# Kernel tuning notes

Measured on AMD Instinct MI355X. Metric: run time of the kernel, lower is better.

The kernel has to match this reference:

```python
import jax, jax.numpy as jnp
import numpy as np

N_NODES = 100000

def spmm(rows, cols, vals, x):
    # out[r] = sum_e vals[e] * x[cols[e]] for edges with rows[e] == r
    msgs = vals[:, None] * x[cols]            # [E, F]
    return jax.ops.segment_sum(msgs, rows, num_segments=N_NODES)

def setup_inputs() -> dict:
    key = jax.random.key(0)
    ks = jax.random.split(key, 8)
    N, E, F_IN, H, C = N_NODES, 1600000, 128, 128, 64
    x = jax.random.normal(ks[0], (N, F_IN), dtype=jnp.float32)
    edge_rows = jax.random.randint(ks[1], (E,), 0, N, dtype=jnp.int32)
    edge_cols = jax.random.randint(ks[2], (E,), 0, N, dtype=jnp.int32)
    edge_vals = jax.random.uniform(ks[3], (E,), dtype=jnp.float32)
    W1 = jax.random.normal(ks[4], (F_IN, H), dtype=jnp.float32) * (1.0 / np.sqrt(F_IN))
    b1 = jnp.zeros((H,), dtype=jnp.float32)
    W2 = jax.random.normal(ks[5], (H, C), dtype=jnp.float32) * (1.0 / np.sqrt(H))
    b2 = jnp.zeros((C,), dtype=jnp.float32)
    return {"x": x, "edge_rows": edge_rows, "edge_cols": edge_cols,
            "edge_vals": edge_vals, "W1": W1, "b1": b1, "W2": W2, "b2": b2}

def reference(x, edge_rows, edge_cols, edge_vals, W1, b1, W2, b2):
    # Layer 1: spmm(adj, x) then linear, then ReLU (dropout = identity at eval)
    h = spmm(edge_rows, edge_cols, edge_vals, x)   # [N, F_IN]
    h = h @ W1 + b1                                # [N, H]
    h = jax.nn.relu(h)
    # Layer 2
    h = spmm(edge_rows, edge_cols, edge_vals, h)   # [N, H]
    return h @ W2 + b2                             # [N, C]
```

## Files before the change

### kernel.cpp

```cpp
#include <hip/hip_runtime.h>


typedef __attribute__((ext_vector_type(8))) short short8;
typedef __attribute__((ext_vector_type(4))) float floatx4;
typedef __attribute__((ext_vector_type(2))) float floatx2;

#define ELLS 64
#define H2LD 136
#define CURS 16

static __device__ __forceinline__ unsigned short f2bf(float f) {
    unsigned int u = __builtin_bit_cast(unsigned int, f);
    u += 0x7fffu + ((u >> 16) & 1u);
    return (unsigned short)(u >> 16);
}
static __device__ __forceinline__ float bflo(unsigned int u) {
    return __builtin_bit_cast(float, u << 16);
}
static __device__ __forceinline__ float bfhi(unsigned int u) {
    return __builtin_bit_cast(float, u & 0xffff0000u);
}
static __device__ __forceinline__ float slotval(unsigned int s) {
    return (float)(s >> 17) * (1.0f / 32767.0f);
}

__global__ __launch_bounds__(256) void prep_kernel(
    const float* __restrict__ W1, const float* __restrict__ W2,
    unsigned short* __restrict__ W1t, unsigned short* __restrict__ W2t,
    int* __restrict__ cursor, int N)
{
    int idx = blockIdx.x * 256 + threadIdx.x;
    int stride = gridDim.x * 256;
    for (int i = idx; i < N * CURS; i += stride) cursor[i] = 0;
    if (idx < 128 * 128) {
        int n = idx >> 7, k = idx & 127;
        W1t[idx] = f2bf(W1[(size_t)k * 128 + n]);
    }
    if (idx < 64 * 128) {
        int n = idx >> 7, k = idx & 127;
        W2t[idx] = f2bf(W2[(size_t)k * 64 + n]);
    }
}

static __device__ __forceinline__ void gemm1_body(
    const float* __restrict__ A, const unsigned short* __restrict__ Wt,
    unsigned short* __restrict__ Y, int N, int bid)
{
    const int lane = threadIdx.x & 63;
    const int wave = threadIdx.x >> 6;
    const int quad = lane >> 4;
    const int l16  = lane & 15;
    const int row0 = bid * 64 + wave * 16;
    int arow = row0 + l16;
    if (arow > N - 1) arow = N - 1;

    short8 af[4];
    const float* ap = A + (size_t)arow * 128 + quad * 8;
    #pragma unroll
    for (int kt = 0; kt < 4; ++kt) {
        const floatx4* p = (const floatx4*)(ap + kt * 32);
        floatx4 lo = __builtin_nontemporal_load(p);
        floatx4 hi = __builtin_nontemporal_load(p + 1);
        short8 t;
        t[0] = (short)f2bf(lo[0]); t[1] = (short)f2bf(lo[1]);
        t[2] = (short)f2bf(lo[2]); t[3] = (short)f2bf(lo[3]);
        t[4] = (short)f2bf(hi[0]); t[5] = (short)f2bf(hi[1]);
        t[6] = (short)f2bf(hi[2]); t[7] = (short)f2bf(hi[3]);
        af[kt] = t;
    }

    floatx4 acc[8];
    #pragma unroll
    for (int nt = 0; nt < 8; ++nt) acc[nt] = (floatx4){0.f, 0.f, 0.f, 0.f};

    #pragma unroll
    for (int nt = 0; nt < 8; ++nt) {
        const unsigned short* wp = Wt + (size_t)(nt * 16 + l16) * 128 + quad * 8;
        #pragma unroll
        for (int kt = 0; kt < 4; ++kt) {
            short8 bfr = *(const short8*)(wp + kt * 32);
            acc[nt] = __builtin_amdgcn_mfma_f32_16x16x32_bf16(
                af[kt], bfr, acc[nt], 0, 0, 0);
        }
    }

    #pragma unroll
    for (int nt = 0; nt < 8; ++nt) {
        int col = nt * 16 + l16;
        #pragma unroll
        for (int r = 0; r < 4; ++r) {
            int row = row0 + quad * 4 + r;
            if (row < N)
                Y[(size_t)row * 128 + col] = f2bf(acc[nt][r]);
        }
    }
}

__global__ __launch_bounds__(256) void fill_ell_gemm1_fused(
    const int* __restrict__ erow, const int* __restrict__ ecol,
    const float* __restrict__ eval, int* __restrict__ cursor,
    unsigned int* __restrict__ ell, int E, int FB, int RSTEP,
    const float* __restrict__ x, const unsigned short* __restrict__ W1t,
    unsigned short* __restrict__ y1b, int N)
{
    if ((int)blockIdx.x < FB) {
        const int g     = blockIdx.x & 7;
        const int chunk = blockIdx.x >> 3;
        const int lo = g * RSTEP;
        const int span = min(RSTEP, N - lo);
        int base = chunk * 1024 + (int)threadIdx.x * 4;
        if (base >= E) return;

        if (base + 4 <= E) {
            int4   r4 = *(const int4*)(erow + base);
            int4   c4 = *(const int4*)(ecol + base);
            float4 v4 = *(const float4*)(eval + base);
            int   rr[4] = {r4.x, r4.y, r4.z, r4.w};
            int   cc[4] = {c4.x, c4.y, c4.z, c4.w};
            float vv[4] = {v4.x, v4.y, v4.z, v4.w};
            #pragma unroll
            for (int j = 0; j < 4; ++j) {
                int r = rr[j];
                if ((unsigned)(r - lo) < (unsigned)span) {
                    int p = atomicAdd(&cursor[(size_t)r * CURS], 1);
                    if (p < ELLS) {
                        unsigned int pk = (unsigned int)cc[j]
                            | ((unsigned int)(int)(vv[j] * 32767.f + 0.5f) << 17);
                        ell[((size_t)r << 6) + p] = pk;
                    }
                }
            }
        } else {
            for (int j = 0; j < 4; ++j) {
                int e = base + j;
                if (e < E) {
                    int r = erow[e];
                    if ((unsigned)(r - lo) < (unsigned)span) {
                        int p = atomicAdd(&cursor[(size_t)r * CURS], 1);
                        if (p < ELLS) {
                            unsigned int pk = (unsigned int)ecol[e]
                                | ((unsigned int)(int)(eval[e] * 32767.f + 0.5f) << 17);
                            ell[((size_t)r << 6) + p] = pk;
                        }
                    }
                }
            }
        }
    } else {
        gemm1_body(x, W1t, y1b, N, blockIdx.x - FB);
    }
}

__global__ __launch_bounds__(1024, 8) void spmm128_gemm2_fused(
    const int* __restrict__ deg, const unsigned int* __restrict__ ell,
    const unsigned short* __restrict__ y1b, const float* __restrict__ b1,
    const unsigned short* __restrict__ W2t,
    unsigned short* __restrict__ y2b, int N)
{
    __shared__ unsigned short h2s[16 * H2LD];

    const int wave = threadIdx.x >> 6;
    const int lane = threadIdx.x & 63;
    const int row  = blockIdx.x * 16 + wave;

    unsigned int pack = 0;
    if (row < N) {
        const unsigned int* xf = (const unsigned int*)y1b;
        int d  = min(deg[(size_t)row * CURS], ELLS);
        int d8 = (d + 7) & ~7;
        const unsigned int* ep = ell + ((size_t)row << 6);

        float ax[8], ay[8];
        #pragma unroll
        for (int j = 0; j < 8; ++j) { ax[j] = 0.f; ay[j] = 0.f; }

        for (int i = 0; i < d8; i += 8) {
            uint4 q0 = *(const uint4*)(ep + i);
            uint4 q1 = *(const uint4*)(ep + i + 4);
            unsigned int s[8] = {q0.x, q0.y, q0.z, q0.w,
                                 q1.x, q1.y, q1.z, q1.w};
            unsigned int sv[8];
            unsigned int u[8];
            #pragma unroll
            for (int j = 0; j < 8; ++j) {
                unsigned int ss = (i + j < d) ? s[j] : 0u;
                sv[j] = ss;
                u[j] = xf[((ss & 0x1FFFFu) << 6) | (unsigned)lane];
            }
            #pragma unroll
            for (int j = 0; j < 8; ++j) {
                float vvv = slotval(sv[j]);
                ax[j] = fmaf(vvv, bflo(u[j]), ax[j]);
                ay[j] = fmaf(vvv, bfhi(u[j]), ay[j]);
            }
        }
        float2 b = ((const float2*)b1)[lane];
        float sx = ((ax[0] + ax[1]) + (ax[2] + ax[3]))
                 + ((ax[4] + ax[5]) + (ax[6] + ax[7])) + b.x;
        float sy = ((ay[0] + ay[1]) + (ay[2] + ay[3]))
                 + ((ay[4] + ay[5]) + (ay[6] + ay[7])) + b.y;
        sx = fmaxf(sx, 0.f);
        sy = fmaxf(sy, 0.f);
        pack = (unsigned int)f2bf(sx) | ((unsigned int)f2bf(sy) << 16);
    }
    ((unsigned int*)(h2s + wave * H2LD))[lane] = pack;
    __syncthreads();

    if (wave < 4) {
        const int quad = lane >> 4;
        const int l16  = lane & 15;
        const int nt   = wave;

        short8 af[4];
        #pragma unroll
        for (int kt = 0; kt < 4; ++kt)
            af[kt] = *(const short8*)(h2s + l16 * H2LD + quad * 8 + kt * 32);

        floatx4 acc = (floatx4){0.f, 0.f, 0.f, 0.f};
        const unsigned short* wp = W2t + (size_t)(nt * 16 + l16) * 128 + quad * 8;
        #pragma unroll
        for (int kt = 0; kt < 4; ++kt) {
            short8 bfr = *(const short8*)(wp + kt * 32);
            acc = __builtin_amdgcn_mfma_f32_16x16x32_bf16(af[kt], bfr, acc, 0, 0, 0);
        }

        int col = nt * 16 + l16;
        #pragma unroll
        for (int r = 0; r < 4; ++r) {
            int grow = blockIdx.x * 16 + quad * 4 + r;
            if (grow < N)
                y2b[(size_t)grow * 64 + col] = f2bf(acc[r]);
        }
    }
}

__global__ __launch_bounds__(256) void spmm_gather64_out(
    const int* __restrict__ deg, const unsigned int* __restrict__ ell,
    const unsigned short* __restrict__ y2b,
    const float* __restrict__ bias, float* __restrict__ out, int N)
{
    int row = (blockIdx.x * 256 + threadIdx.x) >> 6;
    if (row >= N) return;
    int lane = threadIdx.x & 63;
    int half = lane >> 5, fl = lane & 31;
    const unsigned int* xf = (const unsigned int*)y2b;

    int d  = min(deg[(size_t)row * CURS], ELLS);
    int d8 = (d + 7) & ~7;
    const unsigned int* ep = ell + ((size_t)row << 6);

    float ax[4], ay[4];
    #pragma unroll
    for (int j = 0; j < 4; ++j) { ax[j] = 0.f; ay[j] = 0.f; }

    for (int i = half * 4; i < d8; i += 8) {
        uint4 q = *(const uint4*)(ep + i);
        unsigned int s[4] = {q.x, q.y, q.z, q.w};
        unsigned int sv[4];
        unsigned int u[4];
        #pragma unroll
        for (int j = 0; j < 4; ++j) {
            unsigned int ss = (i + j < d) ? s[j] : 0u;
            sv[j] = ss;
            u[j] = xf[((ss & 0x1FFFFu) << 5) | (unsigned)fl];
        }
        #pragma unroll
        for (int j = 0; j < 4; ++j) {
            float vvv = slotval(sv[j]);
            ax[j] = fmaf(vvv, bflo(u[j]), ax[j]);
            ay[j] = fmaf(vvv, bfhi(u[j]), ay[j]);
        }
    }
    float sx = (ax[0] + ax[1]) + (ax[2] + ax[3]);
    float sy = (ay[0] + ay[1]) + (ay[2] + ay[3]);
    sx += __shfl_xor(sx, 32);
    sy += __shfl_xor(sy, 32);
    if (half == 0) {
        float2 b = ((const float2*)bias)[fl];
        floatx2 o; o[0] = sx + b.x; o[1] = sy + b.y;
        __builtin_nontemporal_store(o, (floatx2*)out + (size_t)row * 32 + fl);
    }
}

extern "C" void kernel_launch(void* const* d_in, const int* in_sizes, int n_in,
                              void* d_out, int out_size, void* d_ws, size_t ws_size,
                              hipStream_t stream)
{
    const float* x    = (const float*)d_in[0];
    const int*   erow = (const int*)  d_in[1];
    const int*   ecol = (const int*)  d_in[2];
    const float* eval = (const float*)d_in[3];
    const float* W1   = (const float*)d_in[4];
    const float* b1   = (const float*)d_in[5];
    const float* W2   = (const float*)d_in[6];
    const float* b2   = (const float*)d_in[7];
    float*       out  = (float*)d_out;

    const int N = in_sizes[0] / 128;
    const int E = in_sizes[1];
    const int NP = N + 64;

    unsigned short* y1b = (unsigned short*)d_ws;
    unsigned short* y2b = y1b + (size_t)NP * 128;
    unsigned short* W1t = y2b + (size_t)NP * 64;
    unsigned short* W2t = W1t + 128 * 128;
    unsigned int* ell   = (unsigned int*)(W2t + 64 * 128);
    int*   cursor = (int*)(ell + (size_t)N * ELLS);

    const int spmm_blocks  = (N + 3) / 4;
    const int fused_blocks = (N + 15) / 16;
    const int mfma_blocks  = (N + 63) / 64;
    const int prep_blocks  = (N + 255) / 256;
    const int RSTEP        = (N + 7) / 8;
    const int chunks       = (E + 1023) / 1024;
    const int FB           = 8 * chunks;

    prep_kernel<<<prep_blocks, 256, 0, stream>>>(W1, W2, W1t, W2t, cursor, N);

    fill_ell_gemm1_fused<<<FB + mfma_blocks, 256, 0, stream>>>(
        erow, ecol, eval, cursor, ell, E, FB, RSTEP, x, W1t, y1b, N);

    spmm128_gemm2_fused<<<fused_blocks, 1024, 0, stream>>>(
        cursor, ell, y1b, b1, W2t, y2b, N);

    spmm_gather64_out<<<spmm_blocks, 256, 0, stream>>>(
        cursor, ell, y2b, b2, out, N);
}
```

Baseline: 328.5 us.

## Build ELL via two-pass chunk binning with LDS counting sort instead of global atomics

Replaces the ELL fill, which scanned the edge list eight times and did per-edge global atomics on cursors, with a two-pass binning scheme. Pass A sorts each 4096-edge chunk into 256-row buckets with an LDS histogram and prefix scan, and writes a compact slab plus per-chunk offsets. Pass B has one block per bucket assemble that bucket's ELL rows in LDS and write them out coalesced, along with a dense degree array. This also removes zeroing of the padded cursor array. The cost is an extra kernel launch, an intermediate slab round-trip through memory, and a per-bucket loop over all chunks with limited parallelism.

```diff
diff --git a/kernel.cpp b/kernel.cpp
--- a/kernel.cpp
+++ b/kernel.cpp
@@ -7,7 +7,10 @@
 
 #define ELLS 64
 #define H2LD 136
-#define CURS 16
+#define RW   256
+#define CH   4096
+#define EPT  16
+#define MAXB 400
 
 static __device__ __forceinline__ unsigned short f2bf(float f) {
     unsigned int u = __builtin_bit_cast(unsigned int, f);
@@ -26,12 +29,9 @@
 
 __global__ __launch_bounds__(256) void prep_kernel(
     const float* __restrict__ W1, const float* __restrict__ W2,
-    unsigned short* __restrict__ W1t, unsigned short* __restrict__ W2t,
-    int* __restrict__ cursor, int N)
+    unsigned short* __restrict__ W1t, unsigned short* __restrict__ W2t)
 {
     int idx = blockIdx.x * 256 + threadIdx.x;
-    int stride = gridDim.x * 256;
-    for (int i = idx; i < N * CURS; i += stride) cursor[i] = 0;
     if (idx < 128 * 128) {
         int n = idx >> 7, k = idx & 127;
         W1t[idx] = f2bf(W1[(size_t)k * 128 + n]);
@@ -96,59 +96,143 @@
     }
 }
 
-__global__ __launch_bounds__(256) void fill_ell_gemm1_fused(
+__global__ __launch_bounds__(256) void binA_gemm1_fused(
     const int* __restrict__ erow, const int* __restrict__ ecol,
-    const float* __restrict__ eval, int* __restrict__ cursor,
-    unsigned int* __restrict__ ell, int E, int FB, int RSTEP,
+    const float* __restrict__ eval,
+    uint2* __restrict__ slab, unsigned int* __restrict__ offsT,
+    int E, int NC, int NB,
     const float* __restrict__ x, const unsigned short* __restrict__ W1t,
     unsigned short* __restrict__ y1b, int N)
 {
-    if ((int)blockIdx.x < FB) {
-        const int g     = blockIdx.x & 7;
-        const int chunk = blockIdx.x >> 3;
-        const int lo = g * RSTEP;
-        const int span = min(RSTEP, N - lo);
-        int base = chunk * 1024 + (int)threadIdx.x * 4;
-        if (base >= E) return;
-
-        if (base + 4 <= E) {
-            int4   r4 = *(const int4*)(erow + base);
-            int4   c4 = *(const int4*)(ecol + base);
-            float4 v4 = *(const float4*)(eval + base);
-            int   rr[4] = {r4.x, r4.y, r4.z, r4.w};
-            int   cc[4] = {c4.x, c4.y, c4.z, c4.w};
-            float vv[4] = {v4.x, v4.y, v4.z, v4.w};
+    __shared__ unsigned int hist[MAXB + 1];
+    __shared__ uint2 compact[CH];
+
+    if ((int)blockIdx.x < NC) {
+        const int t     = threadIdx.x;
+        const int chunk = blockIdx.x;
+
+        for (int i = t; i <= NB; i += 256) hist[i] = 0;
+        __syncthreads();
+
+        int base = chunk * CH + t * EPT;
+        unsigned int w0[EPT];
+        unsigned int vb[EPT];
+        int bk[EPT], rk[EPT];
+
+        if (base + EPT <= E) {
             #pragma unroll
-            for (int j = 0; j < 4; ++j) {
-                int r = rr[j];
-                if ((unsigned)(r - lo) < (unsigned)span) {
-                    int p = atomicAdd(&cursor[(size_t)r * CURS], 1);
-                    if (p < ELLS) {
-                        unsigned int pk = (unsigned int)cc[j]
-                            | ((unsigned int)(int)(vv[j] * 32767.f + 0.5f) << 17);
-                        ell[((size_t)r << 6) + p] = pk;
-                    }
+            for (int q = 0; q < 4; ++q) {
+                int4   r4 = *(const int4*)(erow + base + q * 4);
+                int4   c4 = *(const int4*)(ecol + base + q * 4);
+                float4 v4 = *(const float4*)(eval + base + q * 4);
+                int rr[4]   = {r4.x, r4.y, r4.z, r4.w};
+                int cc[4]   = {c4.x, c4.y, c4.z, c4.w};
+                float vv[4] = {v4.x, v4.y, v4.z, v4.w};
+                #pragma unroll
+                for (int j = 0; j < 4; ++j) {
+                    int i = q * 4 + j;
+                    bk[i] = rr[j] >> 8;
+                    w0[i] = (unsigned int)cc[j]
+                          | (((unsigned int)rr[j] & (RW - 1)) << 17);
+                    vb[i] = __builtin_bit_cast(unsigned int, vv[j]);
                 }
             }
         } else {
-            for (int j = 0; j < 4; ++j) {
+            #pragma unroll
+            for (int j = 0; j < EPT; ++j) {
                 int e = base + j;
                 if (e < E) {
                     int r = erow[e];
-                    if ((unsigned)(r - lo) < (unsigned)span) {
-                        int p = atomicAdd(&cursor[(size_t)r * CURS], 1);
-                        if (p < ELLS) {
-                            unsigned int pk = (unsigned int)ecol[e]
-                                | ((unsigned int)(int)(eval[e] * 32767.f + 0.5f) << 17);
-                            ell[((size_t)r << 6) + p] = pk;
-                        }
-                    }
+                    bk[j] = r >> 8;
+                    w0[j] = (unsigned int)ecol[e]
+                          | (((unsigned int)r & (RW - 1)) << 17);
+                    vb[j] = __builtin_bit_cast(unsigned int, eval[e]);
+                } else {
+                    bk[j] = NB;
+                    w0[j] = 0u; vb[j] = 0u;
                 }
             }
         }
+
+        #pragma unroll
+        for (int j = 0; j < EPT; ++j)
+            rk[j] = (int)atomicAdd(&hist[bk[j]], 1u);
+        __syncthreads();
+
+        if (t == 0) {
+            unsigned int run = 0;
+            for (int i = 0; i <= NB; ++i) {
+                unsigned int c = hist[i];
+                hist[i] = run;
+                run += c;
+            }
+        }
+        __syncthreads();
+
+        #pragma unroll
+        for (int j = 0; j < EPT; ++j) {
+            unsigned int pos = hist[bk[j]] + (unsigned int)rk[j];
+            uint2 e; e.x = w0[j]; e.y = vb[j];
+            compact[pos] = e;
+        }
+        __syncthreads();
+
+        uint2* sp = slab + (size_t)chunk * CH;
+        #pragma unroll
+        for (int s = 0; s < EPT; ++s)
+            sp[s * 256 + t] = compact[s * 256 + t];
+        unsigned int* op = offsT + (size_t)chunk * (NB + 1);
+        for (int i = t; i <= NB; i += 256) op[i] = hist[i];
     } else {
-        gemm1_body(x, W1t, y1b, N, blockIdx.x - FB);
-    }
+        gemm1_body(x, W1t, y1b, N, blockIdx.x - NC);
+    }
+}
+
+__global__ __launch_bounds__(256) void binB(
+    const uint2* __restrict__ slab, const unsigned int* __restrict__ offsT,
+    unsigned int* __restrict__ ell, int* __restrict__ deg,
+    int NC, int NB, int N)
+{
+    __shared__ unsigned int ell_lds[RW * ELLS];
+    __shared__ unsigned int cur[RW];
+
+    const int t = threadIdx.x;
+    const int b = blockIdx.x;
+
+    for (int i = t; i < RW; i += 256) cur[i] = 0;
+    __syncthreads();
+
+    const int grp = t >> 5;
+    const int sl  = t & 31;
+    for (int cbase = 0; cbase < NC; cbase += 8) {
+        int c = cbase + grp;
+        if (c < NC) {
+            const unsigned int* op = offsT + (size_t)c * (NB + 1) + b;
+            unsigned int off = op[0];
+            unsigned int end = op[1];
+            const uint2* sp = slab + (size_t)c * CH;
+            for (unsigned int i = off + (unsigned)sl; i < end; i += 32) {
+                uint2 e = sp[i];
+                unsigned int rin = e.x >> 17;
+                unsigned int col = e.x & 0x1FFFFu;
+                float v = __builtin_bit_cast(float, e.y);
+                unsigned int q = (unsigned int)(int)(v * 32767.f + 0.5f);
+                unsigned int p = atomicAdd(&cur[rin], 1u);
+                if (p < ELLS)
+                    ell_lds[rin * ELLS + p] = col | (q << 17);
+            }
+        }
+    }
+    __syncthreads();
+
+    const uint4* src = (const uint4*)ell_lds;
+    uint4* dst = (uint4*)(ell + (size_t)b * RW * ELLS);
+    #pragma unroll
+    for (int s = 0; s < (RW * ELLS / 4) / 256; ++s)
+        dst[s * 256 + t] = src[s * 256 + t];
+
+    int row = b * RW + t;
+    if (row < N) deg[row] = min((int)cur[t], ELLS);
 }
 
 __global__ __launch_bounds__(1024, 8) void spmm128_gemm2_fused(
@@ -166,7 +250,7 @@
     unsigned int pack = 0;
     if (row < N) {
         const unsigned int* xf = (const unsigned int*)y1b;
-        int d  = min(deg[(size_t)row * CURS], ELLS);
+        int d  = min(deg[row], ELLS);
         int d8 = (d + 7) & ~7;
         const unsigned int* ep = ell + ((size_t)row << 6);
 
@@ -245,7 +329,7 @@
     int half = lane >> 5, fl = lane & 31;
     const unsigned int* xf = (const unsigned int*)y2b;
 
-    int d  = min(deg[(size_t)row * CURS], ELLS);
+    int d  = min(deg[row], ELLS);
     int d8 = (d + 7) & ~7;
     const unsigned int* ep = ell + ((size_t)row << 6);
 
@@ -299,30 +383,33 @@
     const int N = in_sizes[0] / 128;
     const int E = in_sizes[1];
     const int NP = N + 64;
+    const int NB = (N + RW - 1) / RW;
+    const int NC = (E + CH - 1) / CH;
 
     unsigned short* y1b = (unsigned short*)d_ws;
     unsigned short* y2b = y1b + (size_t)NP * 128;
     unsigned short* W1t = y2b + (size_t)NP * 64;
     unsigned short* W2t = W1t + 128 * 128;
     unsigned int* ell   = (unsigned int*)(W2t + 64 * 128);
-    int*   cursor = (int*)(ell + (size_t)N * ELLS);
+    uint2* slab         = (uint2*)(ell + (size_t)NB * RW * ELLS);
+    unsigned int* offsT = (unsigned int*)(slab + (size_t)NC * CH);
+    int* deg            = (int*)(offsT + (size_t)NC * (NB + 1));
 
     const int spmm_blocks  = (N + 3) / 4;
     const int fused_blocks = (N + 15) / 16;
     const int mfma_blocks  = (N + 63) / 64;
-    const int prep_blocks  = (N + 255) / 256;
-    const int RSTEP        = (N + 7) / 8;
-    const int chunks       = (E + 1023) / 1024;
-    const int FB           = 8 * chunks;
-
-    prep_kernel<<<prep_blocks, 256, 0, stream>>>(W1, W2, W1t, W2t, cursor, N);
-
-    fill_ell_gemm1_fused<<<FB + mfma_blocks, 256, 0, stream>>>(
-        erow, ecol, eval, cursor, ell, E, FB, RSTEP, x, W1t, y1b, N);
+    const int prep_blocks  = (128 * 128 + 255) / 256;
+
+    prep_kernel<<<prep_blocks, 256, 0, stream>>>(W1, W2, W1t, W2t);
+
+    binA_gemm1_fused<<<NC + mfma_blocks, 256, 0, stream>>>(
+        erow, ecol, eval, slab, offsT, E, NC, NB, x, W1t, y1b, N);
+
+    binB<<<NB, 256, 0, stream>>>(slab, offsT, ell, deg, NC, NB, N);
 
     spmm128_gemm2_fused<<<fused_blocks, 1024, 0, stream>>>(
-        cursor, ell, y1b, b1, W2t, y2b, N);
+        deg, ell, y1b, b1, W2t, y2b, N);
 
     spmm_gather64_out<<<spmm_blocks, 256, 0, stream>>>(
-        cursor, ell, y2b, b2, out, N);
-}
+        deg, ell, y2b, b2, out, N);
+}
```

Result: faster. 299.8 us (-8.7%).
